# Optimization experiments

Hardware: AMD Instinct MI355X
Metric: run time of the kernel (lower is better)

The kernel has to match this reference:

```python
import jax, jax.numpy as jnp
import numpy as np

D = 256; FF = 1024; NH = 8; NL = 4; NP = 4; DH = D // NH
SHAPES = [(64, 64), (32, 32), (16, 16), (8, 8)]
B = 4; N = sum(h * w for h, w in SHAPES)


def _ln(x, g, b, eps=1e-5):
    m = jnp.mean(x, -1, keepdims=True)
    v = jnp.var(x, -1, keepdims=True)
    return (x - m) * jax.lax.rsqrt(v + eps) * g + b


def _bilinear(v, x, y, H, W):
    # v: [B, H*W, nh, dh]; x, y: [B, Nq, nh, P] pixel coords (grid_sample, align_corners=False, zero pad)
    x0 = jnp.floor(x); y0 = jnp.floor(y)
    fx = x - x0; fy = y - y0
    x0 = x0.astype(jnp.int32); y0 = y0.astype(jnp.int32)
    dh = v.shape[-1]
    acc = 0.0
    for xi, yi, w in ((x0, y0, (1 - fx) * (1 - fy)),
                      (x0 + 1, y0, fx * (1 - fy)),
                      (x0, y0 + 1, (1 - fx) * fy),
                      (x0 + 1, y0 + 1, fx * fy)):
        valid = ((xi >= 0) & (xi < W) & (yi >= 0) & (yi < H)).astype(v.dtype)
        idx = jnp.clip(yi, 0, H - 1) * W + jnp.clip(xi, 0, W - 1)  # [B,Nq,nh,P]
        Bq, Nq, nh, P = idx.shape
        idx2 = idx.transpose(0, 1, 3, 2).reshape(Bq, Nq * P, nh, 1)
        idx2 = jnp.broadcast_to(idx2, (Bq, Nq * P, nh, dh))
        g = jnp.take_along_axis(v, idx2, axis=1)  # [B, Nq*P, nh, dh]
        g = g.reshape(Bq, Nq, P, nh, dh).transpose(0, 1, 3, 2, 4)  # [B,Nq,nh,P,dh]
        acc = acc + g * (w * valid)[..., None]
    return acc


def _msdeform(value, loc, attn, shapes):
    # value [B,N,nh,dh]; loc [B,Nq,nh,L,P,2] in [0,1]; attn [B,Nq,nh,L,P]
    out = 0.0; start = 0
    for l, (H, W) in enumerate(shapes):
        v = value[:, start:start + H * W]
        start += H * W
        x = loc[:, :, :, l, :, 0] * W - 0.5
        y = loc[:, :, :, l, :, 1] * H - 0.5
        s = _bilinear(v, x, y, H, W)  # [B,Nq,nh,P,dh]
        out = out + jnp.einsum('bqhpd,bqhp->bqhd', s, attn[:, :, :, l, :])
    return out


def _forward(src, pos, reference_points, w_value, b_value, w_off, b_off, w_attn, b_attn,
             w_out, b_out, g1, be1, w1, b1, w2, b2, g2, be2, padding_mask, shapes):
    q = src + pos
    value = src @ w_value.T + b_value
    value = jnp.where(padding_mask[..., None], 0.0, value).reshape(B, N, NH, DH)
    off = (q @ w_off.T + b_off).reshape(B, N, NH, NL, NP, 2)
    attn = jax.nn.softmax((q @ w_attn.T + b_attn).reshape(B, N, NH, NL * NP), axis=-1)
    attn = attn.reshape(B, N, NH, NL, NP)
    normalizer = jnp.array([[w, h] for h, w in shapes], jnp.float32)  # [L,2] as (W,H)
    loc = reference_points[:, :, None, :, None, :] + off / normalizer[None, None, None, :, None, :]
    a = _msdeform(value, loc, attn, shapes).reshape(B, N, D) @ w_out.T + b_out
    x = _ln(src + a, g1, be1)
    f = jax.nn.relu(x @ w1.T + b1) @ w2.T + b2
    return _ln(x + f, g2, be2)


def setup_inputs() -> dict:
    key = jax.random.key(0)
    ks = iter(jax.random.split(key, 24))
    def p(shape, scale=0.02):
        return jax.random.normal(next(ks), shape, jnp.float32) * scale
    d = {}
    d['src'] = jax.random.normal(next(ks), (B, N, D), jnp.float32)
    d['pos'] = jax.random.normal(next(ks), (B, N, D), jnp.float32)
    d['reference_points'] = jax.random.uniform(next(ks), (B, N, NL, 2), dtype=jnp.float32)
    d['w_value'] = p((D, D)); d['b_value'] = jnp.zeros((D,), jnp.float32)
    d['w_off'] = p((NH * NL * NP * 2, D), 0.001); d['b_off'] = p((NH * NL * NP * 2,), 0.1)
    d['w_attn'] = p((NH * NL * NP, D)); d['b_attn'] = jnp.zeros((NH * NL * NP,), jnp.float32)
    d['w_out'] = p((D, D)); d['b_out'] = jnp.zeros((D,), jnp.float32)
    d['g1'] = jnp.ones((D,), jnp.float32); d['be1'] = jnp.zeros((D,), jnp.float32)
    d['w1'] = p((FF, D)); d['b1'] = jnp.zeros((FF,), jnp.float32)
    d['w2'] = p((D, FF)); d['b2'] = jnp.zeros((D,), jnp.float32)
    d['g2'] = jnp.ones((D,), jnp.float32); d['be2'] = jnp.zeros((D,), jnp.float32)
    d['spatial_shapes'] = jnp.array(SHAPES, jnp.int32)
    d['level_start_index'] = jnp.array(np.cumsum([0] + [h * w for h, w in SHAPES[:-1]]), jnp.int32)
    d['padding_mask'] = jnp.zeros((B, N), bool)
    return d


def reference(src, pos, reference_points, w_value, b_value, w_off, b_off, w_attn, b_attn,
              w_out, b_out, g1, be1, w1, b1, w2, b2, g2, be2,
              spatial_shapes, level_start_index, padding_mask):
    shapes = [tuple(map(int, s)) for s in np.asarray(spatial_shapes)]  # static per-level shapes
    return _forward(src, pos, reference_points, w_value, b_value, w_off, b_off, w_attn, b_attn,
                    w_out, b_out, g1, be1, w1, b1, w2, b2, g2, be2, padding_mask, shapes)
```

## Files before the change

### kernel.cpp

```cpp
#include <hip/hip_runtime.h>

#define B_SZ   4
#define NTOK   5440
#define MTOT   (B_SZ*NTOK)
#define DMODEL 256
#define FFDIM  1024
#define NROWP  (MTOT/128)

typedef __attribute__((ext_vector_type(8))) __bf16 bf16x8;
typedef __attribute__((ext_vector_type(4))) float  f32x4;

static __device__ __forceinline__ unsigned short f2b(float f) {
    unsigned u = __builtin_bit_cast(unsigned, f);
    u = (u + 0x7FFF + ((u >> 16) & 1)) >> 16;
    return (unsigned short)u;
}
static __device__ __forceinline__ float b2f(unsigned short s) {
    return __builtin_bit_cast(float, (unsigned)s << 16);
}
static __device__ __forceinline__ float lo_bf(unsigned u) {
    return __builtin_bit_cast(float, u << 16);
}
static __device__ __forceinline__ float hi_bf(unsigned u) {
    return __builtin_bit_cast(float, u & 0xffff0000u);
}

#define GLL(gp, lp) __builtin_amdgcn_global_load_lds( \
    (const __attribute__((address_space(1))) void*)(gp), \
    (__attribute__((address_space(3))) void*)(lp), 16, 0, 0)

__global__ __launch_bounds__(256)
void qkv_gemm(const unsigned short* __restrict__ src_bf,
              const unsigned short* __restrict__ q_bf,
              const unsigned short* __restrict__ wv_b,
              const unsigned short* __restrict__ woa_b,
              const float* __restrict__ b_value,
              const float* __restrict__ b_off, const float* __restrict__ b_attn,
              const unsigned char* __restrict__ rowmask,
              unsigned short* __restrict__ value_b, unsigned short* __restrict__ oa_b)
{
    const int K = 256;
    const int id  = blockIdx.x;
    const int xcd = id & 7;
    const int j   = id >> 3;
    const int c   = j % 5;
    const int r   = 8 * (j / 5) + xcd;
    if (r >= NROWP) return;
    const int row0 = r * 128;
    const bool isv = (c < 2);
    const unsigned short* A  = isv ? src_bf : q_bf;
    const unsigned short* Wt = isv ? wv_b : woa_b;
    unsigned short* C = isv ? value_b : oa_b;
    const int ldc  = isv ? 256 : 384;
    const int col0 = (isv ? c : (c - 2)) * 128;

    __shared__ unsigned short As[2][128 * 32];
    __shared__ unsigned short Bs[2][128 * 32];
    const int tid  = threadIdx.x;
    const int lane = tid & 63;
    const int wave = tid >> 6;
    const int wr = (wave >> 1) * 64, wc = (wave & 1) * 64;
    const int mrow = lane & 15, quad = lane >> 4;

    f32x4 acc[4][4] = {};
    const int ri0 = tid >> 2,            ki0 = (tid & 3) * 8;
    const int ri1 = (256 + tid) >> 2,    ki1 = ((256 + tid) & 3) * 8;
    const int lds0 = (wave * 64) * 8, lds1 = (256 + wave * 64) * 8;

    for (int k0 = 0; k0 < K; k0 += 64) {
        __syncthreads();
        #pragma unroll
        for (int s = 0; s < 2; ++s) {
            const int kk = k0 + s * 32;
            GLL(A  + (size_t)(row0 + ri0) * K + kk + ki0, &As[s][lds0]);
            GLL(Wt + (size_t)(col0 + ri0) * K + kk + ki0, &Bs[s][lds0]);
            GLL(A  + (size_t)(row0 + ri1) * K + kk + ki1, &As[s][lds1]);
            GLL(Wt + (size_t)(col0 + ri1) * K + kk + ki1, &Bs[s][lds1]);
        }
        __syncthreads();
        #pragma unroll
        for (int s = 0; s < 2; ++s) {
            bf16x8 af[4], bfr[4];
            #pragma unroll
            for (int t4 = 0; t4 < 4; ++t4) {
                af[t4]  = *(const bf16x8*)&As[s][(wr + t4 * 16 + mrow) * 32 + quad * 8];
                bfr[t4] = *(const bf16x8*)&Bs[s][(wc + t4 * 16 + mrow) * 32 + quad * 8];
            }
            #pragma unroll
            for (int ti = 0; ti < 4; ++ti)
                #pragma unroll
                for (int tj = 0; tj < 4; ++tj)
                    acc[ti][tj] = __builtin_amdgcn_mfma_f32_16x16x32_bf16(
                                      bfr[tj], af[ti], acc[ti][tj], 0, 0, 0);
        }
    }

    #pragma unroll
    for (int ti = 0; ti < 4; ++ti) {
        const int row = row0 + wr + ti * 16 + mrow;
        const bool msk = isv && rowmask[row];
        #pragma unroll
        for (int tj = 0; tj < 4; ++tj) {
            const int col = col0 + wc + tj * 16 + quad * 4;
            const float4 bv = isv ? *(const float4*)(b_value + col)
                            : (col < 256 ? *(const float4*)(b_off + col)
                                         : *(const float4*)(b_attn + col - 256));
            ushort4 o;
            o.x = msk ? 0 : f2b(acc[ti][tj][0] + bv.x);
            o.y = msk ? 0 : f2b(acc[ti][tj][1] + bv.y);
            o.z = msk ? 0 : f2b(acc[ti][tj][2] + bv.z);
            o.w = msk ? 0 : f2b(acc[ti][tj][3] + bv.w);
            *(ushort4*)(C + (size_t)row * ldc + col) = o;
        }
    }
}

__global__ __launch_bounds__(256)
void mfma_gemm(const unsigned short* __restrict__ A,
               const unsigned short* __restrict__ Wt,
               const float* __restrict__ bias,
               unsigned short* __restrict__ Cb,
               int Nout, int K)
{
    const int id  = blockIdx.x;
    const int xcd = id & 7;
    const int j   = id >> 3;
    const int ncol = Nout / 128;
    const int c   = j % ncol;
    const int r   = 8 * (j / ncol) + xcd;
    if (r >= NROWP) return;
    const int row0 = r * 128, col0 = c * 128;

    __shared__ unsigned short As[2][128 * 32];
    __shared__ unsigned short Bs[2][128 * 32];
    const int tid  = threadIdx.x;
    const int lane = tid & 63;
    const int wave = tid >> 6;
    const int wr = (wave >> 1) * 64, wc = (wave & 1) * 64;
    const int mrow = lane & 15, quad = lane >> 4;

    f32x4 acc[4][4] = {};
    const int ri0 = tid >> 2,            ki0 = (tid & 3) * 8;
    const int ri1 = (256 + tid) >> 2,    ki1 = ((256 + tid) & 3) * 8;
    const int lds0 = (wave * 64) * 8, lds1 = (256 + wave * 64) * 8;

    for (int k0 = 0; k0 < K; k0 += 64) {
        __syncthreads();
        #pragma unroll
        for (int s = 0; s < 2; ++s) {
            const int kk = k0 + s * 32;
            GLL(A  + (size_t)(row0 + ri0) * K + kk + ki0, &As[s][lds0]);
            GLL(Wt + (size_t)(col0 + ri0) * K + kk + ki0, &Bs[s][lds0]);
            GLL(A  + (size_t)(row0 + ri1) * K + kk + ki1, &As[s][lds1]);
            GLL(Wt + (size_t)(col0 + ri1) * K + kk + ki1, &Bs[s][lds1]);
        }
        __syncthreads();
        #pragma unroll
        for (int s = 0; s < 2; ++s) {
            bf16x8 af[4], bfr[4];
            #pragma unroll
            for (int t4 = 0; t4 < 4; ++t4) {
                af[t4]  = *(const bf16x8*)&As[s][(wr + t4 * 16 + mrow) * 32 + quad * 8];
                bfr[t4] = *(const bf16x8*)&Bs[s][(wc + t4 * 16 + mrow) * 32 + quad * 8];
            }
            #pragma unroll
            for (int ti = 0; ti < 4; ++ti)
                #pragma unroll
                for (int tj = 0; tj < 4; ++tj)
                    acc[ti][tj] = __builtin_amdgcn_mfma_f32_16x16x32_bf16(
                                      bfr[tj], af[ti], acc[ti][tj], 0, 0, 0);
        }
    }

    #pragma unroll
    for (int ti = 0; ti < 4; ++ti) {
        const int row = row0 + wr + ti * 16 + mrow;
        #pragma unroll
        for (int tj = 0; tj < 4; ++tj) {
            const int col = col0 + wc + tj * 16 + quad * 4;
            const float4 bv = *(const float4*)(bias + col);
            ushort4 o;
            o.x = f2b(fmaxf(acc[ti][tj][0] + bv.x, 0.f));
            o.y = f2b(fmaxf(acc[ti][tj][1] + bv.y, 0.f));
            o.z = f2b(fmaxf(acc[ti][tj][2] + bv.z, 0.f));
            o.w = f2b(fmaxf(acc[ti][tj][3] + bv.w, 0.f));
            *(ushort4*)(Cb + (size_t)row * Nout + col) = o;
        }
    }
}

__global__ __launch_bounds__(256)
void gemm_n64(const unsigned short* __restrict__ A,
              const unsigned short* __restrict__ Wt,
              const float* __restrict__ bias,
              unsigned short* __restrict__ Cb,
              int K)
{
    const int id  = blockIdx.x;
    const int xcd = id & 7;
    const int j   = id >> 3;
    const int c   = j % 4;
    const int r   = 8 * (j / 4) + xcd;
    if (r >= NROWP) return;
    const int row0 = r * 128, col0 = c * 64;

    __shared__ unsigned short As[2][128 * 32];
    __shared__ unsigned short Bs[2][64 * 32];
    const int tid  = threadIdx.x;
    const int lane = tid & 63;
    const int wave = tid >> 6;
    const int wr = wave * 32;
    const int mrow = lane & 15, quad = lane >> 4;

    f32x4 acc[2][4] = {};
    const int ri0 = tid >> 2,            ki0 = (tid & 3) * 8;
    const int ri1 = (256 + tid) >> 2,    ki1 = ((256 + tid) & 3) * 8;
    const int ldsA0 = (wave * 64) * 8, ldsA1 = (256 + wave * 64) * 8;
    const int ldsB  = (wave * 64) * 8;

    for (int k0 = 0; k0 < K; k0 += 64) {
        __syncthreads();
        #pragma unroll
        for (int s = 0; s < 2; ++s) {
            const int kk = k0 + s * 32;
            GLL(A  + (size_t)(row0 + ri0) * K + kk + ki0, &As[s][ldsA0]);
            GLL(A  + (size_t)(row0 + ri1) * K + kk + ki1, &As[s][ldsA1]);
            GLL(Wt + (size_t)(col0 + ri0) * K + kk + ki0, &Bs[s][ldsB]);
        }
        __syncthreads();
        #pragma unroll
        for (int s = 0; s < 2; ++s) {
            bf16x8 af[2], bfr[4];
            #pragma unroll
            for (int ti = 0; ti < 2; ++ti)
                af[ti] = *(const bf16x8*)&As[s][(wr + ti * 16 + mrow) * 32 + quad * 8];
            #pragma unroll
            for (int tj = 0; tj < 4; ++tj)
                bfr[tj] = *(const bf16x8*)&Bs[s][(tj * 16 + mrow) * 32 + quad * 8];
            #pragma unroll
            for (int ti = 0; ti < 2; ++ti)
                #pragma unroll
                for (int tj = 0; tj < 4; ++tj)
                    acc[ti][tj] = __builtin_amdgcn_mfma_f32_16x16x32_bf16(
                                      bfr[tj], af[ti], acc[ti][tj], 0, 0, 0);
        }
    }

    #pragma unroll
    for (int ti = 0; ti < 2; ++ti) {
        const int row = row0 + wr + ti * 16 + mrow;
        #pragma unroll
        for (int tj = 0; tj < 4; ++tj) {
            const int col = col0 + tj * 16 + quad * 4;
            const float4 bv = *(const float4*)(bias + col);
            ushort4 o;
            o.x = f2b(acc[ti][tj][0] + bv.x);
            o.y = f2b(acc[ti][tj][1] + bv.y);
            o.z = f2b(acc[ti][tj][2] + bv.z);
            o.w = f2b(acc[ti][tj][3] + bv.w);
            *(ushort4*)(Cb + (size_t)row * 256 + col) = o;
        }
    }
}

__global__ __launch_bounds__(256)
void addln_kernel(const unsigned short* __restrict__ c,
                  const float* __restrict__ resid_f,
                  const unsigned short* __restrict__ resid_b,
                  const float* __restrict__ g, const float* __restrict__ be,
                  float* __restrict__ out_f, unsigned short* __restrict__ out_b)
{
    const int wave = threadIdx.x >> 6;
    const int lane = threadIdx.x & 63;
    const int row  = blockIdx.x * 4 + wave;
    const size_t base = (size_t)row * 256 + (lane << 2);

    const ushort4 cu = *(const ushort4*)(c + base);
    float4 v;
    v.x = b2f(cu.x); v.y = b2f(cu.y); v.z = b2f(cu.z); v.w = b2f(cu.w);
    if (resid_f) {
        const float4 r = *(const float4*)(resid_f + base);
        v.x += r.x; v.y += r.y; v.z += r.z; v.w += r.w;
    } else {
        const ushort4 r = *(const ushort4*)(resid_b + base);
        v.x += b2f(r.x); v.y += b2f(r.y); v.z += b2f(r.z); v.w += b2f(r.w);
    }

    float s  = v.x + v.y + v.z + v.w;
    float ss = v.x * v.x + v.y * v.y + v.z * v.z + v.w * v.w;
    #pragma unroll
    for (int off = 32; off; off >>= 1) {
        s  += __shfl_xor(s, off, 64);
        ss += __shfl_xor(ss, off, 64);
    }
    const float mean = s * (1.f / 256.f);
    const float var  = ss * (1.f / 256.f) - mean * mean;
    const float rstd = rsqrtf(var + 1e-5f);

    const float4 gv = *(const float4*)(g  + (lane << 2));
    const float4 bv = *(const float4*)(be + (lane << 2));
    float4 o;
    o.x = (v.x - mean) * rstd * gv.x + bv.x;
    o.y = (v.y - mean) * rstd * gv.y + bv.y;
    o.z = (v.z - mean) * rstd * gv.z + bv.z;
    o.w = (v.w - mean) * rstd * gv.w + bv.w;
    if (out_f) *(float4*)(out_f + base) = o;
    if (out_b) {
        ushort4 u; u.x = f2b(o.x); u.y = f2b(o.y); u.z = f2b(o.z); u.w = f2b(o.w);
        *(ushort4*)(out_b + base) = u;
    }
}

__global__ __launch_bounds__(256)
void sampling_kernel(const unsigned short* __restrict__ value,
                     const unsigned short* __restrict__ oa,
                     const float* __restrict__ refp,
                     unsigned short* __restrict__ samp)
{
    __shared__ unsigned s_pk[64 * 68];
    const int t0  = blockIdx.x * 8;
    const int tid = threadIdx.x;

    #pragma unroll
    for (int rep = 0; rep < 4; ++rep) {
        const int e   = rep * 256 + tid;
        const int tok = e >> 7;
        const int hp  = e & 127;
        const int h   = hp >> 4, i16 = hp & 15, l = i16 >> 2;
        const int t   = t0 + tok;

        const float ex = __expf(b2f(oa[(size_t)t * 384 + 256 + h * 16 + i16]));
        float ssum = ex;
        #pragma unroll
        for (int o = 8; o; o >>= 1) ssum += __shfl_xor(ssum, o, 16);
        const float aw = ex / ssum;

        const int   Wl_t[4]  = {64, 32, 16, 8};
        const int   LST_t[4] = {0, 4096, 5120, 5376};
        const int   Wl  = Wl_t[l];
        const int   LST = LST_t[l];
        const float fW  = (float)Wl;

        const unsigned ov = *(const unsigned*)&oa[(size_t)t * 384 + h * 32 + i16 * 2];
        const float ox = lo_bf(ov), oy = hi_bf(ov);
        const float2 rxy = *(const float2*)&refp[(size_t)t * 8 + l * 2];
        const float x = rxy.x * fW + ox - 0.5f;
        const float y = rxy.y * fW + oy - 0.5f;
        const float x0 = floorf(x), y0 = floorf(y);
        const float fx = x - x0, fy = y - y0;
        const int   ix = (int)x0, iy = (int)y0;
        const bool  vx0 = (ix >= 0) & (ix < Wl), vx1 = (ix + 1 >= 0) & (ix + 1 < Wl);

        const int base = (tok * 8 + h) * 68 + i16 * 4;
        #pragma unroll
        for (int j = 0; j < 2; ++j) {
            const int  yv = iy + j;
            const bool vy = (yv >= 0) & (yv < Wl);
            const float wy = (j ? fy : 1.f - fy) * aw;
            const int  rowi = LST + yv * Wl;
            const float w0 = (vy & vx0) ? wy * (1.f - fx) : 0.f;
            const float w1 = (vy & vx1) ? wy * fx : 0.f;
            const unsigned i0 = (vy & vx0) ? (unsigned)(rowi + ix) : 0u;
            const unsigned i1 = (vy & vx1) ? (unsigned)(rowi + ix + 1) : 0u;
            s_pk[base + j * 2 + 0] = (i0 << 16) | f2b(w0);
            s_pk[base + j * 2 + 1] = (i1 << 16) | f2b(w1);
        }
    }
    __syncthreads();

    const int wv_  = tid >> 6;
    const int lane = tid & 63;
    const int t2   = lane >> 5;
    const int h    = (lane >> 2) & 7;
    const int dq   = lane & 3;
    const int tok  = wv_ * 2 + t2;
    const int t    = t0 + tok;
    const int b    = t / NTOK;
    const char* vb = (const char*)value + ((size_t)b * NTOK * 256 + h * 32 + dq * 8) * 2;
    const unsigned* sp = s_pk + (tok * 8 + h) * 68;

    float a0 = 0.f, a1 = 0.f, a2 = 0.f, a3 = 0.f;
    float a4 = 0.f, a5 = 0.f, a6 = 0.f, a7 = 0.f;

    unsigned pkc = sp[0];
    uint4 vc = *(const uint4*)(vb + (size_t)(pkc >> 16) * 512);
    #pragma unroll 8
    for (int i = 0; i < 64; ++i) {
        unsigned pkn = 0; uint4 vn = make_uint4(0, 0, 0, 0);
        if (i < 63) {
            pkn = sp[i + 1];
            vn = *(const uint4*)(vb + (size_t)(pkn >> 16) * 512);
        }
        const float w = lo_bf(pkc);
        a0 += lo_bf(vc.x) * w; a1 += hi_bf(vc.x) * w;
        a2 += lo_bf(vc.y) * w; a3 += hi_bf(vc.y) * w;
        a4 += lo_bf(vc.z) * w; a5 += hi_bf(vc.z) * w;
        a6 += lo_bf(vc.w) * w; a7 += hi_bf(vc.w) * w;
        pkc = pkn; vc = vn;
    }
    ushort4 o0, o1;
    o0.x = f2b(a0); o0.y = f2b(a1); o0.z = f2b(a2); o0.w = f2b(a3);
    o1.x = f2b(a4); o1.y = f2b(a5); o1.z = f2b(a6); o1.w = f2b(a7);
    unsigned short* op = samp + (size_t)t * 256 + h * 32 + dq * 8;
    *(ushort4*)(op)     = o0;
    *(ushort4*)(op + 4) = o1;
}

__global__ __launch_bounds__(256)
void prep_kernel(const float* __restrict__ src, const float* __restrict__ pos,
                 const float* __restrict__ wv, const float* __restrict__ woff,
                 const float* __restrict__ wattn, const float* __restrict__ wout,
                 const float* __restrict__ w1, const float* __restrict__ w2,
                 unsigned short* __restrict__ q_bf, unsigned short* __restrict__ src_bf,
                 unsigned short* __restrict__ wv_b, unsigned short* __restrict__ woa_b,
                 unsigned short* __restrict__ wout_b,
                 unsigned short* __restrict__ w1_b, unsigned short* __restrict__ w2_b)
{
    const int v = blockIdx.x * 256 + threadIdx.x;
    if (v < 1392640) {
        const float4 s = ((const float4*)src)[v];
        const float4 p = ((const float4*)pos)[v];
        ushort4 qo, so;
        qo.x = f2b(s.x + p.x); qo.y = f2b(s.y + p.y);
        qo.z = f2b(s.z + p.z); qo.w = f2b(s.w + p.w);
        so.x = f2b(s.x); so.y = f2b(s.y); so.z = f2b(s.z); so.w = f2b(s.w);
        ((ushort4*)q_bf)[v]   = qo;
        ((ushort4*)src_bf)[v] = so;
        return;
    }
    const int v2 = v - 1392640;
    const float* s; unsigned short* d; int off;
    if      (v2 <  16384) { s = wv;    d = wv_b;          off = v2; }
    else if (v2 <  32768) { s = woff;  d = woa_b;         off = v2 - 16384; }
    else if (v2 <  40960) { s = wattn; d = woa_b + 65536; off = v2 - 32768; }
    else if (v2 <  57344) { s = wout;  d = wout_b;        off = v2 - 40960; }
    else if (v2 < 122880) { s = w1;    d = w1_b;          off = v2 - 57344; }
    else                  { s = w2;    d = w2_b;          off = v2 - 122880; }
    const float4 f = ((const float4*)s)[off];
    ushort4 u; u.x = f2b(f.x); u.y = f2b(f.y); u.z = f2b(f.z); u.w = f2b(f.w);
    ((ushort4*)d)[off] = u;
}

extern "C" void kernel_launch(void* const* d_in, const int* in_sizes, int n_in,
                              void* d_out, int out_size, void* d_ws, size_t ws_size,
                              hipStream_t stream) {
    const float* src     = (const float*)d_in[0];
    const float* pos     = (const float*)d_in[1];
    const float* refp    = (const float*)d_in[2];
    const float* w_value = (const float*)d_in[3];
    const float* b_value = (const float*)d_in[4];
    const float* w_off   = (const float*)d_in[5];
    const float* b_off   = (const float*)d_in[6];
    const float* w_attn  = (const float*)d_in[7];
    const float* b_attn  = (const float*)d_in[8];
    const float* w_out   = (const float*)d_in[9];
    const float* b_out   = (const float*)d_in[10];
    const float* g1      = (const float*)d_in[11];
    const float* be1     = (const float*)d_in[12];
    const float* w1      = (const float*)d_in[13];
    const float* b1      = (const float*)d_in[14];
    const float* w2      = (const float*)d_in[15];
    const float* b2      = (const float*)d_in[16];
    const float* g2      = (const float*)d_in[17];
    const float* be2     = (const float*)d_in[18];
    const unsigned char* pmask = (const unsigned char*)d_in[21];

    char* ws = (char*)d_ws;
    const size_t SZ16 = (size_t)MTOT * 256 * 2;
    unsigned short* q_bf    = (unsigned short*)(ws);
    unsigned short* src_bf  = (unsigned short*)(ws + SZ16);
    unsigned short* value_b = (unsigned short*)(ws + 2 * SZ16);
    unsigned short* oa_b    = (unsigned short*)(ws + 3 * SZ16);
    unsigned short* samp    = (unsigned short*)(ws + 3 * SZ16 + SZ16 * 3 / 2);
    unsigned short* h_bf    = (unsigned short*)(ws + 5 * SZ16 + SZ16 * 3 / 2);
    unsigned short* wts     = (unsigned short*)(ws + 9 * SZ16 + SZ16 * 3 / 2);
    unsigned short* C1_bf   = (unsigned short*)(ws + 2 * SZ16);
    unsigned short* x_bf    = (unsigned short*)(ws);
    unsigned short* C2_bf   = samp;

    unsigned short* wv_b    = wts;
    unsigned short* woa_b   = wv_b   + 65536;
    unsigned short* wout_b  = woa_b  + 98304;
    unsigned short* w1_b    = wout_b + 65536;
    unsigned short* w2_b    = w1_b   + 262144;

    const dim3 blk(256);

    prep_kernel<<<dim3(6176), blk, 0, stream>>>(src, pos, w_value, w_off, w_attn,
                                                w_out, w1, w2, q_bf, src_bf,
                                                wv_b, woa_b, wout_b, w1_b, w2_b);
    qkv_gemm<<<dim3(8 * 5 * 22), blk, 0, stream>>>(
        src_bf, q_bf, wv_b, woa_b, b_value, b_off, b_attn, pmask, value_b, oa_b);
    sampling_kernel<<<dim3(MTOT / 8), blk, 0, stream>>>(value_b, oa_b, refp, samp);
    gemm_n64<<<dim3(8 * 4 * 22), blk, 0, stream>>>(
        samp, wout_b, b_out, C1_bf, DMODEL);
    addln_kernel<<<dim3(MTOT / 4), blk, 0, stream>>>(
        C1_bf, src, nullptr, g1, be1, nullptr, x_bf);
    mfma_gemm<<<dim3(8 * 8 * 22), blk, 0, stream>>>(
        x_bf, w1_b, b1, h_bf, FFDIM, DMODEL);
    gemm_n64<<<dim3(8 * 4 * 22), blk, 0, stream>>>(
        h_bf, w2_b, b2, C2_bf, FFDIM);
    addln_kernel<<<dim3(MTOT / 4), blk, 0, stream>>>(
        C2_bf, nullptr, x_bf, g2, be2, (float*)d_out, nullptr);
}
```

Before: 273.7 us.

## Fuse fp32-to-bf16 conversion into GEMM loads and drop prep kernel

Removes the separate prep kernel that converted src, src+pos and all weights to bf16. The GEMMs now read fp32 through registers, add pos where needed, convert, and store into double-buffered LDS with a register prefetch of the next k-slice. This replaces global_load_lds with register staging. The sampling loop is also restructured to batch eight gathers before accumulating. The change saves one full pass over activations and one launch, but the GEMMs re-read fp32 weights per block and do conversion ALU work.

```diff
diff --git a/kernel.cpp b/kernel.cpp
--- a/kernel.cpp
+++ b/kernel.cpp
@@ -24,16 +24,20 @@
 static __device__ __forceinline__ float hi_bf(unsigned u) {
     return __builtin_bit_cast(float, u & 0xffff0000u);
 }
-
-#define GLL(gp, lp) __builtin_amdgcn_global_load_lds( \
-    (const __attribute__((address_space(1))) void*)(gp), \
-    (__attribute__((address_space(3))) void*)(lp), 16, 0, 0)
+static __device__ __forceinline__ unsigned pk2(float lo, float hi) {
+    return (unsigned)f2b(lo) | ((unsigned)f2b(hi) << 16);
+}
+static __device__ __forceinline__ uint4 cvt8(const float4 a, const float4 b) {
+    uint4 u;
+    u.x = pk2(a.x, a.y); u.y = pk2(a.z, a.w);
+    u.z = pk2(b.x, b.y); u.w = pk2(b.z, b.w);
+    return u;
+}
 
 __global__ __launch_bounds__(256)
-void qkv_gemm(const unsigned short* __restrict__ src_bf,
-              const unsigned short* __restrict__ q_bf,
-              const unsigned short* __restrict__ wv_b,
-              const unsigned short* __restrict__ woa_b,
+void qkv_gemm(const float* __restrict__ src, const float* __restrict__ pos,
+              const float* __restrict__ w_value, const float* __restrict__ w_off,
+              const float* __restrict__ w_attn,
               const float* __restrict__ b_value,
               const float* __restrict__ b_off, const float* __restrict__ b_attn,
               const unsigned char* __restrict__ rowmask,
@@ -48,11 +52,13 @@
     if (r >= NROWP) return;
     const int row0 = r * 128;
     const bool isv = (c < 2);
-    const unsigned short* A  = isv ? src_bf : q_bf;
-    const unsigned short* Wt = isv ? wv_b : woa_b;
+    const float* Wp;
+    int col0;
+    if (isv)          { Wp = w_value + (size_t)(c * 128) * 256;       col0 = c * 128; }
+    else if (c < 4)   { Wp = w_off   + (size_t)((c - 2) * 128) * 256; col0 = (c - 2) * 128; }
+    else              { Wp = w_attn;                                  col0 = 256; }
     unsigned short* C = isv ? value_b : oa_b;
-    const int ldc  = isv ? 256 : 384;
-    const int col0 = (isv ? c : (c - 2)) * 128;
+    const int ldc = isv ? 256 : 384;
 
     __shared__ unsigned short As[2][128 * 32];
     __shared__ unsigned short Bs[2][128 * 32];
@@ -62,37 +68,60 @@
     const int wr = (wave >> 1) * 64, wc = (wave & 1) * 64;
     const int mrow = lane & 15, quad = lane >> 4;
 
+    const int ri = tid >> 1, ki = (tid & 1) * 16;
+    const float* Ap = src + (size_t)(row0 + ri) * 256 + ki;
+    const float* Pp = pos + (size_t)(row0 + ri) * 256 + ki;
+    const float* Bp = Wp  + (size_t)ri * 256 + ki;
+
     f32x4 acc[4][4] = {};
-    const int ri0 = tid >> 2,            ki0 = (tid & 3) * 8;
-    const int ri1 = (256 + tid) >> 2,    ki1 = ((256 + tid) & 3) * 8;
-    const int lds0 = (wave * 64) * 8, lds1 = (256 + wave * 64) * 8;
-
-    for (int k0 = 0; k0 < K; k0 += 64) {
+    float4 a[4], b[4];
+
+    #pragma unroll
+    for (int q = 0; q < 4; ++q) {
+        a[q] = ((const float4*)Ap)[q];
+        b[q] = ((const float4*)Bp)[q];
+    }
+    if (!isv) {
+        #pragma unroll
+        for (int q = 0; q < 4; ++q) {
+            const float4 p = ((const float4*)Pp)[q];
+            a[q].x += p.x; a[q].y += p.y; a[q].z += p.z; a[q].w += p.w;
+        }
+    }
+
+    int ib = 0;
+    for (int k0 = 0; k0 < K; k0 += 32, ib ^= 1) {
+        *(uint4*)&As[ib][ri * 32 + ki]     = cvt8(a[0], a[1]);
+        *(uint4*)&As[ib][ri * 32 + ki + 8] = cvt8(a[2], a[3]);
+        *(uint4*)&Bs[ib][ri * 32 + ki]     = cvt8(b[0], b[1]);
+        *(uint4*)&Bs[ib][ri * 32 + ki + 8] = cvt8(b[2], b[3]);
         __syncthreads();
-        #pragma unroll
-        for (int s = 0; s < 2; ++s) {
-            const int kk = k0 + s * 32;
-            GLL(A  + (size_t)(row0 + ri0) * K + kk + ki0, &As[s][lds0]);
-            GLL(Wt + (size_t)(col0 + ri0) * K + kk + ki0, &Bs[s][lds0]);
-            GLL(A  + (size_t)(row0 + ri1) * K + kk + ki1, &As[s][lds1]);
-            GLL(Wt + (size_t)(col0 + ri1) * K + kk + ki1, &Bs[s][lds1]);
-        }
-        __syncthreads();
-        #pragma unroll
-        for (int s = 0; s < 2; ++s) {
-            bf16x8 af[4], bfr[4];
+        if (k0 + 32 < K) {
             #pragma unroll
-            for (int t4 = 0; t4 < 4; ++t4) {
-                af[t4]  = *(const bf16x8*)&As[s][(wr + t4 * 16 + mrow) * 32 + quad * 8];
-                bfr[t4] = *(const bf16x8*)&Bs[s][(wc + t4 * 16 + mrow) * 32 + quad * 8];
+            for (int q = 0; q < 4; ++q) {
+                a[q] = ((const float4*)(Ap + k0 + 32))[q];
+                b[q] = ((const float4*)(Bp + k0 + 32))[q];
             }
+            if (!isv) {
+                #pragma unroll
+                for (int q = 0; q < 4; ++q) {
+                    const float4 p = ((const float4*)(Pp + k0 + 32))[q];
+                    a[q].x += p.x; a[q].y += p.y; a[q].z += p.z; a[q].w += p.w;
+                }
+            }
+        }
+        bf16x8 af[4], bfr[4];
+        #pragma unroll
+        for (int t4 = 0; t4 < 4; ++t4) {
+            af[t4]  = *(const bf16x8*)&As[ib][(wr + t4 * 16 + mrow) * 32 + quad * 8];
+            bfr[t4] = *(const bf16x8*)&Bs[ib][(wc + t4 * 16 + mrow) * 32 + quad * 8];
+        }
+        #pragma unroll
+        for (int ti = 0; ti < 4; ++ti)
             #pragma unroll
-            for (int ti = 0; ti < 4; ++ti)
-                #pragma unroll
-                for (int tj = 0; tj < 4; ++tj)
-                    acc[ti][tj] = __builtin_amdgcn_mfma_f32_16x16x32_bf16(
-                                      bfr[tj], af[ti], acc[ti][tj], 0, 0, 0);
-        }
+            for (int tj = 0; tj < 4; ++tj)
+                acc[ti][tj] = __builtin_amdgcn_mfma_f32_16x16x32_bf16(
+                                  bfr[tj], af[ti], acc[ti][tj], 0, 0, 0);
     }
 
     #pragma unroll
@@ -116,18 +145,16 @@
 }
 
 __global__ __launch_bounds__(256)
-void mfma_gemm(const unsigned short* __restrict__ A,
-               const unsigned short* __restrict__ Wt,
-               const float* __restrict__ bias,
-               unsigned short* __restrict__ Cb,
-               int Nout, int K)
+void ffn1_gemm(const unsigned short* __restrict__ A,
+               const float* __restrict__ W, const float* __restrict__ bias,
+               unsigned short* __restrict__ Cb)
 {
+    const int K = 256, Nout = 1024;
     const int id  = blockIdx.x;
     const int xcd = id & 7;
     const int j   = id >> 3;
-    const int ncol = Nout / 128;
-    const int c   = j % ncol;
-    const int r   = 8 * (j / ncol) + xcd;
+    const int c   = j & 7;
+    const int r   = 8 * (j >> 3) + xcd;
     if (r >= NROWP) return;
     const int row0 = r * 128, col0 = c * 128;
 
@@ -139,37 +166,41 @@
     const int wr = (wave >> 1) * 64, wc = (wave & 1) * 64;
     const int mrow = lane & 15, quad = lane >> 4;
 
+    const int ri = tid >> 1, ki = (tid & 1) * 16;
+    const unsigned short* Ap = A + (size_t)(row0 + ri) * K + ki;
+    const float* Bp = W + (size_t)(col0 + ri) * K + ki;
+
     f32x4 acc[4][4] = {};
-    const int ri0 = tid >> 2,            ki0 = (tid & 3) * 8;
-    const int ri1 = (256 + tid) >> 2,    ki1 = ((256 + tid) & 3) * 8;
-    const int lds0 = (wave * 64) * 8, lds1 = (256 + wave * 64) * 8;
-
-    for (int k0 = 0; k0 < K; k0 += 64) {
+    uint4 ua0, ua1; float4 b[4];
+    ua0 = ((const uint4*)Ap)[0]; ua1 = ((const uint4*)Ap)[1];
+    #pragma unroll
+    for (int q = 0; q < 4; ++q) b[q] = ((const float4*)Bp)[q];
+
+    int ib = 0;
+    for (int k0 = 0; k0 < K; k0 += 32, ib ^= 1) {
+        *(uint4*)&As[ib][ri * 32 + ki]     = ua0;
+        *(uint4*)&As[ib][ri * 32 + ki + 8] = ua1;
+        *(uint4*)&Bs[ib][ri * 32 + ki]     = cvt8(b[0], b[1]);
+        *(uint4*)&Bs[ib][ri * 32 + ki + 8] = cvt8(b[2], b[3]);
         __syncthreads();
-        #pragma unroll
-        for (int s = 0; s < 2; ++s) {
-            const int kk = k0 + s * 32;
-            GLL(A  + (size_t)(row0 + ri0) * K + kk + ki0, &As[s][lds0]);
-            GLL(Wt + (size_t)(col0 + ri0) * K + kk + ki0, &Bs[s][lds0]);
-            GLL(A  + (size_t)(row0 + ri1) * K + kk + ki1, &As[s][lds1]);
-            GLL(Wt + (size_t)(col0 + ri1) * K + kk + ki1, &Bs[s][lds1]);
-        }
-        __syncthreads();
-        #pragma unroll
-        for (int s = 0; s < 2; ++s) {
-            bf16x8 af[4], bfr[4];
+        if (k0 + 32 < K) {
+            ua0 = ((const uint4*)(Ap + k0 + 32))[0];
+            ua1 = ((const uint4*)(Ap + k0 + 32))[1];
             #pragma unroll
-            for (int t4 = 0; t4 < 4; ++t4) {
-                af[t4]  = *(const bf16x8*)&As[s][(wr + t4 * 16 + mrow) * 32 + quad * 8];
-                bfr[t4] = *(const bf16x8*)&Bs[s][(wc + t4 * 16 + mrow) * 32 + quad * 8];
-            }
+            for (int q = 0; q < 4; ++q) b[q] = ((const float4*)(Bp + k0 + 32))[q];
+        }
+        bf16x8 af[4], bfr[4];
+        #pragma unroll
+        for (int t4 = 0; t4 < 4; ++t4) {
+            af[t4]  = *(const bf16x8*)&As[ib][(wr + t4 * 16 + mrow) * 32 + quad * 8];
+            bfr[t4] = *(const bf16x8*)&Bs[ib][(wc + t4 * 16 + mrow) * 32 + quad * 8];
+        }
+        #pragma unroll
+        for (int ti = 0; ti < 4; ++ti)
             #pragma unroll
-            for (int ti = 0; ti < 4; ++ti)
-                #pragma unroll
-                for (int tj = 0; tj < 4; ++tj)
-                    acc[ti][tj] = __builtin_amdgcn_mfma_f32_16x16x32_bf16(
-                                      bfr[tj], af[ti], acc[ti][tj], 0, 0, 0);
-        }
+            for (int tj = 0; tj < 4; ++tj)
+                acc[ti][tj] = __builtin_amdgcn_mfma_f32_16x16x32_bf16(
+                                  bfr[tj], af[ti], acc[ti][tj], 0, 0, 0);
     }
 
     #pragma unroll
@@ -191,16 +222,14 @@
 
 __global__ __launch_bounds__(256)
 void gemm_n64(const unsigned short* __restrict__ A,
-              const unsigned short* __restrict__ Wt,
-              const float* __restrict__ bias,
-              unsigned short* __restrict__ Cb,
-              int K)
+              const float* __restrict__ W, const float* __restrict__ bias,
+              unsigned short* __restrict__ Cb, int K)
 {
     const int id  = blockIdx.x;
     const int xcd = id & 7;
     const int j   = id >> 3;
-    const int c   = j % 4;
-    const int r   = 8 * (j / 4) + xcd;
+    const int c   = j & 3;
+    const int r   = 8 * (j >> 2) + xcd;
     if (r >= NROWP) return;
     const int row0 = r * 128, col0 = c * 64;
 
@@ -212,38 +241,41 @@
     const int wr = wave * 32;
     const int mrow = lane & 15, quad = lane >> 4;
 
+    const int ri = tid >> 1, ki = (tid & 1) * 16;
+    const int rb = tid >> 2, kb = (tid & 3) * 8;
+    const unsigned short* Ap = A + (size_t)(row0 + ri) * K + ki;
+    const float* Bp = W + (size_t)(col0 + rb) * K + kb;
+
     f32x4 acc[2][4] = {};
-    const int ri0 = tid >> 2,            ki0 = (tid & 3) * 8;
-    const int ri1 = (256 + tid) >> 2,    ki1 = ((256 + tid) & 3) * 8;
-    const int ldsA0 = (wave * 64) * 8, ldsA1 = (256 + wave * 64) * 8;
-    const int ldsB  = (wave * 64) * 8;
-
-    for (int k0 = 0; k0 < K; k0 += 64) {
+    uint4 ua0, ua1; float4 b0, b1;
+    ua0 = ((const uint4*)Ap)[0]; ua1 = ((const uint4*)Ap)[1];
+    b0 = ((const float4*)Bp)[0]; b1 = ((const float4*)Bp)[1];
+
+    int ib = 0;
+    for (int k0 = 0; k0 < K; k0 += 32, ib ^= 1) {
+        *(uint4*)&As[ib][ri * 32 + ki]     = ua0;
+        *(uint4*)&As[ib][ri * 32 + ki + 8] = ua1;
+        *(uint4*)&Bs[ib][rb * 32 + kb]     = cvt8(b0, b1);
         __syncthreads();
-        #pragma unroll
-        for (int s = 0; s < 2; ++s) {
-            const int kk = k0 + s * 32;
-            GLL(A  + (size_t)(row0 + ri0) * K + kk + ki0, &As[s][ldsA0]);
-            GLL(A  + (size_t)(row0 + ri1) * K + kk + ki1, &As[s][ldsA1]);
-            GLL(Wt + (size_t)(col0 + ri0) * K + kk + ki0, &Bs[s][ldsB]);
-        }
-        __syncthreads();
-        #pragma unroll
-        for (int s = 0; s < 2; ++s) {
-            bf16x8 af[2], bfr[4];
-            #pragma unroll
-            for (int ti = 0; ti < 2; ++ti)
-                af[ti] = *(const bf16x8*)&As[s][(wr + ti * 16 + mrow) * 32 + quad * 8];
+        if (k0 + 32 < K) {
+            ua0 = ((const uint4*)(Ap + k0 + 32))[0];
+            ua1 = ((const uint4*)(Ap + k0 + 32))[1];
+            b0 = ((const float4*)(Bp + k0 + 32))[0];
+            b1 = ((const float4*)(Bp + k0 + 32))[1];
+        }
+        bf16x8 af[2], bfr[4];
+        #pragma unroll
+        for (int ti = 0; ti < 2; ++ti)
+            af[ti] = *(const bf16x8*)&As[ib][(wr + ti * 16 + mrow) * 32 + quad * 8];
+        #pragma unroll
+        for (int tj = 0; tj < 4; ++tj)
+            bfr[tj] = *(const bf16x8*)&Bs[ib][(tj * 16 + mrow) * 32 + quad * 8];
+        #pragma unroll
+        for (int ti = 0; ti < 2; ++ti)
             #pragma unroll
             for (int tj = 0; tj < 4; ++tj)
-                bfr[tj] = *(const bf16x8*)&Bs[s][(tj * 16 + mrow) * 32 + quad * 8];
-            #pragma unroll
-            for (int ti = 0; ti < 2; ++ti)
-                #pragma unroll
-                for (int tj = 0; tj < 4; ++tj)
-                    acc[ti][tj] = __builtin_amdgcn_mfma_f32_16x16x32_bf16(
-                                      bfr[tj], af[ti], acc[ti][tj], 0, 0, 0);
-        }
+                acc[ti][tj] = __builtin_amdgcn_mfma_f32_16x16x32_bf16(
+                                  bfr[tj], af[ti], acc[ti][tj], 0, 0, 0);
     }
 
     #pragma unroll
@@ -353,17 +385,17 @@
 
         const int base = (tok * 8 + h) * 68 + i16 * 4;
         #pragma unroll
-        for (int j = 0; j < 2; ++j) {
-            const int  yv = iy + j;
+        for (int jj = 0; jj < 2; ++jj) {
+            const int  yv = iy + jj;
             const bool vy = (yv >= 0) & (yv < Wl);
-            const float wy = (j ? fy : 1.f - fy) * aw;
+            const float wy = (jj ? fy : 1.f - fy) * aw;
             const int  rowi = LST + yv * Wl;
             const float w0 = (vy & vx0) ? wy * (1.f - fx) : 0.f;
             const float w1 = (vy & vx1) ? wy * fx : 0.f;
             const unsigned i0 = (vy & vx0) ? (unsigned)(rowi + ix) : 0u;
             const unsigned i1 = (vy & vx1) ? (unsigned)(rowi + ix + 1) : 0u;
-            s_pk[base + j * 2 + 0] = (i0 << 16) | f2b(w0);
-            s_pk[base + j * 2 + 1] = (i1 << 16) | f2b(w1);
+            s_pk[base + jj * 2 + 0] = (i0 << 16) | f2b(w0);
+            s_pk[base + jj * 2 + 1] = (i1 << 16) | f2b(w1);
         }
     }
     __syncthreads();
@@ -382,21 +414,23 @@
     float a0 = 0.f, a1 = 0.f, a2 = 0.f, a3 = 0.f;
     float a4 = 0.f, a5 = 0.f, a6 = 0.f, a7 = 0.f;
 
-    unsigned pkc = sp[0];
-    uint4 vc = *(const uint4*)(vb + (size_t)(pkc >> 16) * 512);
-    #pragma unroll 8
-    for (int i = 0; i < 64; ++i) {
-        unsigned pkn = 0; uint4 vn = make_uint4(0, 0, 0, 0);
-        if (i < 63) {
-            pkn = sp[i + 1];
-            vn = *(const uint4*)(vb + (size_t)(pkn >> 16) * 512);
-        }
-        const float w = lo_bf(pkc);
-        a0 += lo_bf(vc.x) * w; a1 += hi_bf(vc.x) * w;
-        a2 += lo_bf(vc.y) * w; a3 += hi_bf(vc.y) * w;
-        a4 += lo_bf(vc.z) * w; a5 += hi_bf(vc.z) * w;
-        a6 += lo_bf(vc.w) * w; a7 += hi_bf(vc.w) * w;
-        pkc = pkn; vc = vn;
+    #pragma unroll
+    for (int g = 0; g < 8; ++g) {
+        unsigned pk[8];
+        #pragma unroll
+        for (int jj = 0; jj < 8; ++jj) pk[jj] = sp[g * 8 + jj];
+        uint4 vv[8];
+        #pragma unroll
+        for (int jj = 0; jj < 8; ++jj)
+            vv[jj] = *(const uint4*)(vb + (size_t)(pk[jj] >> 16) * 512);
+        #pragma unroll
+        for (int jj = 0; jj < 8; ++jj) {
+            const float w = lo_bf(pk[jj]);
+            a0 += lo_bf(vv[jj].x) * w; a1 += hi_bf(vv[jj].x) * w;
+            a2 += lo_bf(vv[jj].y) * w; a3 += hi_bf(vv[jj].y) * w;
+            a4 += lo_bf(vv[jj].z) * w; a5 += hi_bf(vv[jj].z) * w;
+            a6 += lo_bf(vv[jj].w) * w; a7 += hi_bf(vv[jj].w) * w;
+        }
     }
     ushort4 o0, o1;
     o0.x = f2b(a0); o0.y = f2b(a1); o0.z = f2b(a2); o0.w = f2b(a3);
@@ -404,41 +438,6 @@
     unsigned short* op = samp + (size_t)t * 256 + h * 32 + dq * 8;
     *(ushort4*)(op)     = o0;
     *(ushort4*)(op + 4) = o1;
-}
-
-__global__ __launch_bounds__(256)
-void prep_kernel(const float* __restrict__ src, const float* __restrict__ pos,
-                 const float* __restrict__ wv, const float* __restrict__ woff,
-                 const float* __restrict__ wattn, const float* __restrict__ wout,
-                 const float* __restrict__ w1, const float* __restrict__ w2,
-                 unsigned short* __restrict__ q_bf, unsigned short* __restrict__ src_bf,
-                 unsigned short* __restrict__ wv_b, unsigned short* __restrict__ woa_b,
-                 unsigned short* __restrict__ wout_b,
-                 unsigned short* __restrict__ w1_b, unsigned short* __restrict__ w2_b)
-{
-    const int v = blockIdx.x * 256 + threadIdx.x;
-    if (v < 1392640) {
-        const float4 s = ((const float4*)src)[v];
-        const float4 p = ((const float4*)pos)[v];
-        ushort4 qo, so;
-        qo.x = f2b(s.x + p.x); qo.y = f2b(s.y + p.y);
-        qo.z = f2b(s.z + p.z); qo.w = f2b(s.w + p.w);
-        so.x = f2b(s.x); so.y = f2b(s.y); so.z = f2b(s.z); so.w = f2b(s.w);
-        ((ushort4*)q_bf)[v]   = qo;
-        ((ushort4*)src_bf)[v] = so;
-        return;
-    }
-    const int v2 = v - 1392640;
-    const float* s; unsigned short* d; int off;
-    if      (v2 <  16384) { s = wv;    d = wv_b;          off = v2; }
-    else if (v2 <  32768) { s = woff;  d = woa_b;         off = v2 - 16384; }
-    else if (v2 <  40960) { s = wattn; d = woa_b + 65536; off = v2 - 32768; }
-    else if (v2 <  57344) { s = wout;  d = wout_b;        off = v2 - 40960; }
-    else if (v2 < 122880) { s = w1;    d = w1_b;          off = v2 - 57344; }
-    else                  { s = w2;    d = w2_b;          off = v2 - 122880; }
-    const float4 f = ((const float4*)s)[off];
-    ushort4 u; u.x = f2b(f.x); u.y = f2b(f.y); u.z = f2b(f.z); u.w = f2b(f.w);
-    ((ushort4*)d)[off] = u;
 }
 
 extern "C" void kernel_launch(void* const* d_in, const int* in_sizes, int n_in,
@@ -466,40 +465,27 @@
     const unsigned char* pmask = (const unsigned char*)d_in[21];
 
     char* ws = (char*)d_ws;
-    const size_t SZ16 = (size_t)MTOT * 256 * 2;
-    unsigned short* q_bf    = (unsigned short*)(ws);
-    unsigned short* src_bf  = (unsigned short*)(ws + SZ16);
-    unsigned short* value_b = (unsigned short*)(ws + 2 * SZ16);
-    unsigned short* oa_b    = (unsigned short*)(ws + 3 * SZ16);
-    unsigned short* samp    = (unsigned short*)(ws + 3 * SZ16 + SZ16 * 3 / 2);
-    unsigned short* h_bf    = (unsigned short*)(ws + 5 * SZ16 + SZ16 * 3 / 2);
-    unsigned short* wts     = (unsigned short*)(ws + 9 * SZ16 + SZ16 * 3 / 2);
-    unsigned short* C1_bf   = (unsigned short*)(ws + 2 * SZ16);
-    unsigned short* x_bf    = (unsigned short*)(ws);
+    const size_t SZ16  = (size_t)MTOT * 256 * 2;
+    const size_t SZ384 = (size_t)MTOT * 384 * 2;
+    unsigned short* value_b = (unsigned short*)(ws);
+    unsigned short* oa_b    = (unsigned short*)(ws + SZ16);
+    unsigned short* samp    = (unsigned short*)(ws + SZ16 + SZ384);
+    unsigned short* h_bf    = (unsigned short*)(ws + 2 * SZ16 + SZ384);
+    unsigned short* C1_bf   = value_b;
+    unsigned short* x_bf    = oa_b;
     unsigned short* C2_bf   = samp;
 
-    unsigned short* wv_b    = wts;
-    unsigned short* woa_b   = wv_b   + 65536;
-    unsigned short* wout_b  = woa_b  + 98304;
-    unsigned short* w1_b    = wout_b + 65536;
-    unsigned short* w2_b    = w1_b   + 262144;
-
     const dim3 blk(256);
 
-    prep_kernel<<<dim3(6176), blk, 0, stream>>>(src, pos, w_value, w_off, w_attn,
-                                                w_out, w1, w2, q_bf, src_bf,
-                                                wv_b, woa_b, wout_b, w1_b, w2_b);
     qkv_gemm<<<dim3(8 * 5 * 22), blk, 0, stream>>>(
-        src_bf, q_bf, wv_b, woa_b, b_value, b_off, b_attn, pmask, value_b, oa_b);
+        src, pos, w_value, w_off, w_attn, b_value, b_off, b_attn, pmask,
+        value_b, oa_b);
     sampling_kernel<<<dim3(MTOT / 8), blk, 0, stream>>>(value_b, oa_b, refp, samp);
-    gemm_n64<<<dim3(8 * 4 * 22), blk, 0, stream>>>(
-        samp, wout_b, b_out, C1_bf, DMODEL);
+    gemm_n64<<<dim3(8 * 4 * 22), blk, 0, stream>>>(samp, w_out, b_out, C1_bf, DMODEL);
     addln_kernel<<<dim3(MTOT / 4), blk, 0, stream>>>(
         C1_bf, src, nullptr, g1, be1, nullptr, x_bf);
-    mfma_gemm<<<dim3(8 * 8 * 22), blk, 0, stream>>>(
-        x_bf, w1_b, b1, h_bf, FFDIM, DMODEL);
-    gemm_n64<<<dim3(8 * 4 * 22), blk, 0, stream>>>(
-        h_bf, w2_b, b2, C2_bf, FFDIM);
+    ffn1_gemm<<<dim3(8 * 8 * 22), blk, 0, stream>>>(x_bf, w1, b1, h_bf);
+    gemm_n64<<<dim3(8 * 4 * 22), blk, 0, stream>>>(h_bf, w2, b2, C2_bf, FFDIM);
     addln_kernel<<<dim3(MTOT / 4), blk, 0, stream>>>(
         C2_bf, nullptr, x_bf, g2, be2, (float*)d_out, nullptr);
 }
```

Result: slower. 293.0 us (+7.1%).
